# Optimization experiments

Hardware: AMD Instinct MI355X
Metric: run time of the kernel (lower is better)

Reference implementation:

```python
import jax, jax.numpy as jnp
import numpy as np

B, N, D, C = 256, 4096, 128, 32

def setup_inputs() -> dict:
    key = jax.random.key(0)
    k1, k2, k3, k4 = jax.random.split(key, 4)
    queries = jax.random.normal(k1, (B, D), dtype=jnp.float32)
    cases = jax.random.normal(k2, (N, D), dtype=jnp.float32)
    targets = jax.random.normal(k3, (N, C), dtype=jnp.float32)
    feature_weights = jnp.ones((N, D), dtype=jnp.float32)
    distance_weights = jax.random.normal(k4, (N, D), dtype=jnp.float32) * 0.05 - 0.15
    ca_bias = jnp.zeros((N,), dtype=jnp.float32)
    return {
        "queries": queries, "cases": cases, "targets": targets,
        "feature_weights": feature_weights,
        "distance_weights": distance_weights,
        "ca_bias": ca_bias,
    }

def reference(queries, cases, targets, feature_weights, distance_weights, ca_bias):
    # delta: [B, N, D] weighted squared distance per feature
    fw = jax.nn.softplus(feature_weights)                       # [N, D]
    delta = (queries[:, None, :] - cases[None, :, :]) ** 2 * fw[None, :, :]
    # case activations: weighted reduce over D, then sigmoid gate
    w = -jnp.abs(distance_weights)                              # [N, D]
    case_act = jnp.sum(delta * w[None, :, :], axis=2) + ca_bias[None, :]  # [B, N]
    activations = jax.nn.sigmoid(case_act)
    # target adaptation: normalized weighted aggregation of targets
    ca_norm = activations / (jnp.sum(activations, axis=1, keepdims=True) + 0.01)
    y_hat = ca_norm @ targets                                   # [B, C]
    return (y_hat, activations, delta)
```

## Files before the change

### kernel.cpp

```cpp
#include <hip/hip_runtime.h>
#include <math.h>

#define B_ 256
#define N_ 4096
#define D_ 128
#define C_ 32

typedef float vf4 __attribute__((ext_vector_type(4)));

__global__ __launch_bounds__(256) void prep_kernel(
    const float* __restrict__ fwin, const float* __restrict__ dwin,
    const float* __restrict__ cases, const float* __restrict__ bias,
    float* __restrict__ fwsp, float* __restrict__ w1t,
    float* __restrict__ w2t, float* __restrict__ t3) {
  const int g = threadIdx.x >> 5;
  const int lane = threadIdx.x & 31;
  const int n = blockIdx.x * 8 + g;
  const int d0 = lane * 4;
  const size_t off = (size_t)n * D_ + d0;

  const vf4 x = *(const vf4*)(fwin + off);
  const vf4 w = *(const vf4*)(dwin + off);
  const vf4 c = *(const vf4*)(cases + off);

  vf4 sp, wfw, m2;
  float s = 0.f;
  #pragma unroll
  for (int k = 0; k < 4; ++k) {
    const float xv = x[k];
    const float spk = (xv > 20.f) ? xv : log1pf(expf(xv));
    const float wk = spk * (-fabsf(w[k]));
    sp[k] = spk;
    wfw[k] = wk;
    m2[k] = -2.f * c[k] * wk;
    s += c[k] * c[k] * wk;
  }
  *(vf4*)(fwsp + off) = sp;
  #pragma unroll
  for (int k = 0; k < 4; ++k) {
    w1t[(size_t)(d0 + k) * N_ + n] = wfw[k];
    w2t[(size_t)(d0 + k) * N_ + n] = m2[k];
  }
  #pragma unroll
  for (int o = 16; o > 0; o >>= 1)
    s += __shfl_xor(s, o, 32);
  if (lane == 0) t3[n] = s + bias[n];
}

__global__ __launch_bounds__(256) void delta_kernel(
    const float* __restrict__ q,
    const float* __restrict__ cases,
    const float* __restrict__ fwsp,
    float* __restrict__ delta_out) {
  const int nc   = blockIdx.x & 255;
  const int bc   = blockIdx.x >> 8;
  const int g    = threadIdx.x >> 5;
  const int lane = threadIdx.x & 31;
  const int d0   = lane * 4;
  const int b0   = bc * 32;

  int n[2];
  vf4 cv[2], fv[2];
  n[0] = nc * 16 + g;
  n[1] = n[0] + 8;
  #pragma unroll
  for (int j = 0; j < 2; ++j) {
    const size_t off = (size_t)n[j] * D_ + d0;
    cv[j] = *(const vf4*)(cases + off);
    fv[j] = *(const vf4*)(fwsp + off);
  }

  #pragma unroll 4
  for (int bi = 0; bi < 32; ++bi) {
    const int b = b0 + bi;
    const vf4 qv = *(const vf4*)(q + (size_t)b * D_ + d0);
    #pragma unroll
    for (int j = 0; j < 2; ++j) {
      const vf4 dd = qv - cv[j];
      const vf4 dl = (dd * dd) * fv[j];
      __builtin_nontemporal_store(
          dl, (vf4*)(delta_out + ((size_t)b * N_ + n[j]) * D_ + d0));
    }
  }
}

__global__ __launch_bounds__(256) void act_kernel(
    const float* __restrict__ q,
    const float* __restrict__ w1t,
    const float* __restrict__ w2t,
    const float* __restrict__ t3,
    float* __restrict__ act) {
  const int bc = blockIdx.x >> 4;
  const int nc = blockIdx.x & 15;
  const int kq = threadIdx.x >> 6;
  const int nl = threadIdx.x & 63;
  const int n0 = nc * 256 + nl * 4;
  const int b0 = bc * 8;

  vf4 acc[8];
  #pragma unroll
  for (int b = 0; b < 8; ++b) acc[b] = (vf4)(0.f);

  #pragma unroll 4
  for (int kk = 0; kk < 32; ++kk) {
    const int k = kq * 32 + kk;
    const vf4 w1 = *(const vf4*)(w1t + (size_t)k * N_ + n0);
    const vf4 w2 = *(const vf4*)(w2t + (size_t)k * N_ + n0);
    #pragma unroll
    for (int b = 0; b < 8; ++b) {
      const float a = q[(size_t)(b0 + b) * D_ + k];
      acc[b] += (a * a) * w1 + a * w2;
    }
  }

  __shared__ vf4 part[3][8][64];
  if (kq > 0) {
    #pragma unroll
    for (int b = 0; b < 8; ++b) part[kq - 1][b][nl] = acc[b];
  }
  __syncthreads();
  if (kq == 0) {
    const vf4 tv = *(const vf4*)(t3 + n0);
    #pragma unroll
    for (int t = 0; t < 3; ++t)
      #pragma unroll
      for (int b = 0; b < 8; ++b) acc[b] += part[t][b][nl];
    #pragma unroll
    for (int b = 0; b < 8; ++b) {
      const vf4 ca = acc[b] + tv;
      vf4 av;
      #pragma unroll
      for (int k = 0; k < 4; ++k)
        av[k] = 1.f / (1.f + __expf(-ca[k]));
      *(vf4*)(act + (size_t)(b0 + b) * N_ + n0) = av;
    }
  }
}

__global__ __launch_bounds__(1024) void finish_kernel(
    const float* __restrict__ act,
    const float* __restrict__ targets,
    float* __restrict__ y) {
  const int b = blockIdx.x;
  const int c = threadIdx.x & 31;
  const int g = threadIdx.x >> 5;
  float ys = 0.f, ss = 0.f;
  for (int n0 = g * 4; n0 < N_; n0 += 128) {
    const vf4 a = *(const vf4*)(act + (size_t)b * N_ + n0);
    ys += a.x * targets[(size_t)(n0 + 0) * C_ + c];
    ys += a.y * targets[(size_t)(n0 + 1) * C_ + c];
    ys += a.z * targets[(size_t)(n0 + 2) * C_ + c];
    ys += a.w * targets[(size_t)(n0 + 3) * C_ + c];
    ss += (a.x + a.y) + (a.z + a.w);
  }
  __shared__ float sm_y[32][33];
  __shared__ float sm_s[32];
  sm_y[g][c] = ys;
  if (c == 0) sm_s[g] = ss;
  __syncthreads();
  if (g == 0) {
    float t = 0.f, s = 0.f;
    #pragma unroll
    for (int k = 0; k < 32; ++k) { t += sm_y[k][c]; s += sm_s[k]; }
    y[(size_t)b * C_ + c] = t / (s + 0.01f);
  }
}

extern "C" void kernel_launch(void* const* d_in, const int* in_sizes, int n_in,
                              void* d_out, int out_size, void* d_ws, size_t ws_size,
                              hipStream_t stream) {
  const float* queries = (const float*)d_in[0];
  const float* cases   = (const float*)d_in[1];
  const float* targets = (const float*)d_in[2];
  const float* fwin    = (const float*)d_in[3];
  const float* dwin    = (const float*)d_in[4];
  const float* bias    = (const float*)d_in[5];

  float* out   = (float*)d_out;
  float* y_hat = out;
  float* act   = out + (size_t)B_ * C_;
  float* delta = act + (size_t)B_ * N_;

  float* fwsp = (float*)d_ws;
  float* w1t  = fwsp + (size_t)N_ * D_;
  float* w2t  = w1t + (size_t)D_ * N_;
  float* t3   = w2t + (size_t)D_ * N_;

  prep_kernel<<<N_ / 8, 256, 0, stream>>>(fwin, dwin, cases, bias,
                                          fwsp, w1t, w2t, t3);
  delta_kernel<<<2048, 256, 0, stream>>>(queries, cases, fwsp, delta);
  act_kernel<<<512, 256, 0, stream>>>(queries, w1t, w2t, t3, act);
  finish_kernel<<<B_, 1024, 0, stream>>>(act, targets, y_hat);
}
```

Before: 581.6 us.

## Restructure delta kernel as grid-stride flat stores with regular stores

Rewrites the delta kernel so that each thread owns one (n, d-chunk) of the case/weight data and walks over the batch dimension in a grid-stride pattern. The whole grid then writes a contiguous flat slice of the output on each iteration. The nontemporal store builtin is replaced with a plain store. The aim is to make the write stream perfectly linear across the device and to cut index arithmetic. The trade-off is fewer cases reused per thread, and writes may now pollute the cache.

```diff
diff --git a/kernel.cpp b/kernel.cpp
--- a/kernel.cpp
+++ b/kernel.cpp
@@ -52,35 +52,23 @@
     const float* __restrict__ cases,
     const float* __restrict__ fwsp,
     float* __restrict__ delta_out) {
-  const int nc   = blockIdx.x & 255;
-  const int bc   = blockIdx.x >> 8;
-  const int g    = threadIdx.x >> 5;
-  const int lane = threadIdx.x & 31;
-  const int d0   = lane * 4;
-  const int b0   = bc * 32;
+  const unsigned tid = blockIdx.x * 256u + threadIdx.x;
+  const unsigned r   = tid & 131071u;
+  const unsigned n   = r >> 5;
+  const unsigned d0  = (r & 31u) << 2;
 
-  int n[2];
-  vf4 cv[2], fv[2];
-  n[0] = nc * 16 + g;
-  n[1] = n[0] + 8;
-  #pragma unroll
-  for (int j = 0; j < 2; ++j) {
-    const size_t off = (size_t)n[j] * D_ + d0;
-    cv[j] = *(const vf4*)(cases + off);
-    fv[j] = *(const vf4*)(fwsp + off);
-  }
+  const vf4 cv = *(const vf4*)(cases + ((size_t)n << 7) + d0);
+  const vf4 fv = *(const vf4*)(fwsp  + ((size_t)n << 7) + d0);
 
+  unsigned b = tid >> 17;
+  float* outp = delta_out + ((size_t)tid << 2);
   #pragma unroll 4
-  for (int bi = 0; bi < 32; ++bi) {
-    const int b = b0 + bi;
-    const vf4 qv = *(const vf4*)(q + (size_t)b * D_ + d0);
-    #pragma unroll
-    for (int j = 0; j < 2; ++j) {
-      const vf4 dd = qv - cv[j];
-      const vf4 dl = (dd * dd) * fv[j];
-      __builtin_nontemporal_store(
-          dl, (vf4*)(delta_out + ((size_t)b * N_ + n[j]) * D_ + d0));
-    }
+  for (int s = 0; s < 64; ++s) {
+    const vf4 qv = *(const vf4*)(q + ((size_t)b << 7) + d0);
+    const vf4 dd = qv - cv;
+    *(vf4*)outp = (dd * dd) * fv;
+    b += 4u;
+    outp += (size_t)524288u * 4u;
   }
 }
 
```

Result: slower. 601.4 us (+3.4%).
